# Kernel optimization log

Hardware: AMD Instinct MI355X
Metric: run time of the kernel (lower is better)

The kernel has to match this reference:

```python
import jax, jax.numpy as jnp
import numpy as np

STRIDE = 1
PAD = 1

def setup_inputs() -> dict:
    key = jax.random.key(0)
    k1, k2 = jax.random.split(key)
    x = jax.random.normal(k1, (32, 128, 56, 56), dtype=jnp.float32)
    W = jax.random.normal(k2, (256, 128, 3, 3), dtype=jnp.float32)
    b = jnp.zeros((256,), dtype=jnp.float32)
    return {"x": x, "W": W, "b": b}

def reference(x, W, b):
    # Faithful conv2d: NCHW input, OIHW weight, stride 1, pad 1, plus bias.
    out = jax.lax.conv_general_dilated(
        x, W,
        window_strides=(STRIDE, STRIDE),
        padding=((PAD, PAD), (PAD, PAD)),
        dimension_numbers=("NCHW", "OIHW", "NCHW"),
    )
    return out + b[None, :, None, None]
```

## Files before the change

kernel.cpp:

```cpp
#include <hip/hip_runtime.h>
#include <hip/hip_bf16.h>
#include <cstdint>
#include <cstddef>

#define NB   32
#define CIN  128
#define HWP  3136
#define KOC  256
#define NRS  9
#define PROW 3364
#define WINR 384
#define AEL  12288

typedef __attribute__((ext_vector_type(8))) short  short8;
typedef __attribute__((ext_vector_type(4))) short  short4v;
typedef __attribute__((ext_vector_type(4))) float  float4v;

__device__ __forceinline__ unsigned short f2bf(float f) {
    union { float f; unsigned int u; } v; v.f = f;
    unsigned int u = v.u;
    u = u + 0x7fffu + ((u >> 16) & 1u);
    return (unsigned short)(u >> 16);
}

__global__ __launch_bounds__(256) void prep_kernel(const float* __restrict__ W,
                                                   unsigned short* __restrict__ wt2,
                                                   const float* __restrict__ x,
                                                   unsigned short* __restrict__ xt) {
    __shared__ unsigned short lds[32 * 260];
    int blk = blockIdx.x;
    int t   = threadIdx.x;

    if (blk < 1152) {
        int idx  = blk * 256 + t;
        int e    = idx & 7;
        int lr   = (idx >> 3) & 15;
        int quad = (idx >> 7) & 3;
        int i    = (idx >> 9) & 3;
        int wm   = (idx >> 11) & 1;
        int rem  = idx >> 12;
        int s    = rem % 3;
        int q    = rem / 3;
        int ot   = q & 1;
        int r    = (q >> 1) % 3;
        int ck   = q / 6;
        int rs   = r * 3 + s;
        int oc = ot * 128 + wm * 64 + i * 16 + lr;
        int c  = ck * 32 + quad * 8 + e;
        wt2[idx] = f2bf(W[((size_t)oc * CIN + c) * NRS + rs]);
        return;
    }

    if (blk >= 2816) {
        int g = (blk - 2816) * 256 + t;
        int slab = g / 228;
        int gi   = g - slab * 228;
        int row;
        if (gi < 59)       row = gi;
        else if (gi < 169) { int k = gi - 59;
                             row = 115 + 58 * (k >> 1) + (k & 1); }
        else               row = 3305 + (gi - 169);
        unsigned short* gr = xt + (size_t)slab * (PROW * 32) + (size_t)row * 32;
        short8 z = (short8)0;
        *(short8*)(gr +  0) = z;
        *(short8*)(gr +  8) = z;
        *(short8*)(gr + 16) = z;
        *(short8*)(gr + 24) = z;
        return;
    }

    int b    = blk - 1152;
    int tile = b % 13;
    int ck   = (b / 13) & 3;
    int n    = b / 52;
    int hw0  = tile * 256;
    int wv   = t >> 6;
    int lane = t & 63;

    const float* src = x + ((size_t)(n * CIN + ck * 32)) * HWP;
    #pragma unroll
    for (int pass = 0; pass < 8; ++pass) {
        int c  = pass * 4 + wv;
        int hw = hw0 + lane * 4;
        if (hw < HWP) {
            float4v v = *(const float4v*)(src + (size_t)c * HWP + hw);
            short4v s4;
            #pragma unroll
            for (int k = 0; k < 4; ++k) s4[k] = (short)f2bf(v[k]);
            *(short4v*)(&lds[c * 260 + lane * 4]) = s4;
        }
    }
    __syncthreads();

    int sub = t & 3;
    int hwl = t >> 2;
    unsigned short* dst = xt + ((size_t)(n * 4 + ck)) * PROW * 32;
    #pragma unroll
    for (int pass = 0; pass < 4; ++pass) {
        int hl = pass * 64 + hwl;
        int hw = hw0 + hl;
        if (hw < HWP) {
            short8 v;
            #pragma unroll
            for (int j = 0; j < 8; ++j)
                v[j] = (short)lds[(sub * 8 + j) * 260 + hl];
            int pr = hw + 59 + 2 * (hw / 56);
            *(short8*)(dst + (size_t)pr * 32 + sub * 8) = v;
        }
    }
}

__device__ __forceinline__ void stage_A(const unsigned short* src,
                                        unsigned short* lbase,
                                        int wv, int lane) {
    #pragma unroll
    for (int it = 0; it < 3; ++it) {
        int c0 = it * 512 + wv * 64;
        __builtin_amdgcn_global_load_lds(
            (const __attribute__((address_space(1))) void*)(src + (size_t)(c0 + lane) * 8),
            (__attribute__((address_space(3))) void*)(lbase + (size_t)c0 * 8), 16, 0, 0);
    }
}

__device__ __forceinline__ void stage_B(const unsigned short* gwin,
                                        unsigned short* lbase,
                                        int wv, int lane) {
    #pragma unroll
    for (int it = 0; it < 3; ++it) {
        int blk = it * 8 + wv;
        int s   = blk * 64 + lane;
        int r   = s >> 2;
        int q   = s & 3;
        int qs  = q ^ ((r >> 1) & 3);
        __builtin_amdgcn_global_load_lds(
            (const __attribute__((address_space(1))) void*)(gwin + r * 32 + qs * 8),
            (__attribute__((address_space(3))) void*)(lbase + (size_t)blk * 512), 16, 0, 0);
    }
}

__device__ __forceinline__ short8 ldb(const char* lb, int r, int quad) {
    int q = quad ^ ((r >> 1) & 3);
    return *(const short8*)(lb + r * 64 + q * 16);
}

__global__ __launch_bounds__(512, 2) void gemm_kernel(const unsigned short* __restrict__ xt,
                                                      const unsigned short* __restrict__ wt2,
                                                      const float* __restrict__ bias,
                                                      float* __restrict__ out) {
    __shared__ unsigned short lds[49152];

    int bx = blockIdx.x;
    int ot = bx & 1;
    int n  = (bx >> 1) & 31;
    int pt = bx >> 6;
    int p0 = pt * 256;

    int t    = threadIdx.x;
    int wv   = t >> 6;
    int lane = t & 63;
    int lr   = lane & 15;
    int quad = lane >> 4;
    int wm   = wv >> 2;
    int wn   = wv & 3;

    int prbase = p0 + 2 * (p0 / 56);

    int rb[4];
    #pragma unroll
    for (int j = 0; j < 4; ++j) {
        int hw  = p0 + wn * 64 + j * 16 + lr;
        int hwc = hw < HWP ? hw : (HWP - 1);
        rb[j] = hwc + 59 + 2 * (hwc / 56) - prbase;
    }

    const unsigned short* xb = xt + (size_t)n * 4 * PROW * 32;
    const unsigned short* wb = wt2 + ot * AEL;

    float4v acc[4][4];
    #pragma unroll
    for (int i = 0; i < 4; ++i)
        #pragma unroll
        for (int j = 0; j < 4; ++j)
            acc[i][j] = (float4v){0.f, 0.f, 0.f, 0.f};

    stage_A(wb, lds, wv, lane);
    stage_B(xb + (size_t)prbase * 32, lds + 24576, wv, lane);
    __syncthreads();

    for (int ck = 0; ck < 4; ++ck) {
        for (int r = 0; r < 3; ++r) {
            int g = ck * 3 + r;
            if (g < 11) {
                int r2  = (r == 2) ? 0 : r + 1;
                int ck2 = (r == 2) ? ck + 1 : ck;
                stage_A(wb + (size_t)ck2 * 73728 + (size_t)r2 * 24576,
                        lds + ((g + 1) & 1) * AEL, wv, lane);
            }
            if (r == 2 && ck < 3)
                stage_B(xb + (size_t)(ck + 1) * (PROW * 32) + (size_t)prbase * 32,
                        lds + 24576 + ((ck + 1) & 1) * AEL, wv, lane);

            const unsigned short* A = lds + (g & 1) * AEL + wm * 2048 + lane * 8;
            const char* lbB = (const char*)(lds + 24576 + (ck & 1) * AEL);
            int sh0 = (r - 1) * 58;

            #pragma unroll
            for (int s = 0; s < 3; ++s) {
                int shift = sh0 + s - 1;
                short8 af[4];
                #pragma unroll
                for (int i = 0; i < 4; ++i)
                    af[i] = *(const short8*)(A + s * 4096 + i * 512);
                short8 bcur = ldb(lbB, rb[0] + shift, quad);
                #pragma unroll
                for (int j = 0; j < 4; ++j) {
                    short8 bnext;
                    if (j < 3) bnext = ldb(lbB, rb[j + 1] + shift, quad);
                    #pragma unroll
                    for (int i = 0; i < 4; ++i)
                        acc[i][j] = __builtin_amdgcn_mfma_f32_16x16x32_bf16(
                            af[i], bcur, acc[i][j], 0, 0, 0);
                    if (j < 3) bcur = bnext;
                }
            }
            __syncthreads();
        }
    }

    float* orow = out + (size_t)n * KOC * HWP;
    #pragma unroll
    for (int i = 0; i < 4; ++i) {
        #pragma unroll
        for (int rr = 0; rr < 4; ++rr) {
            int oc = ot * 128 + wm * 64 + i * 16 + quad * 4 + rr;
            float bi = bias[oc];
            #pragma unroll
            for (int j = 0; j < 4; ++j) {
                int hw = p0 + wn * 64 + j * 16 + lr;
                if (hw < HWP)
                    orow[(size_t)oc * HWP + hw] = acc[i][j][rr] + bi;
            }
        }
    }
}

__global__ void naive_kernel(const float* __restrict__ x, const float* __restrict__ W,
                             const float* __restrict__ b, float* __restrict__ out) {
    size_t idx = (size_t)blockIdx.x * 256 + threadIdx.x;
    if (idx >= (size_t)NB * KOC * HWP) return;
    int w0 = (int)(idx % 56);
    int h0 = (int)((idx / 56) % 56);
    int k  = (int)((idx / HWP) % KOC);
    int n  = (int)(idx / ((size_t)HWP * KOC));
    float acc = b[k];
    for (int c = 0; c < CIN; ++c) {
        const float* xr = x + ((size_t)n * CIN + c) * HWP;
        const float* wr = W + ((size_t)k * CIN + c) * NRS;
        for (int r = 0; r < 3; ++r) {
            int h = h0 + r - 1;
            if ((unsigned)h >= 56u) continue;
            for (int s = 0; s < 3; ++s) {
                int w = w0 + s - 1;
                if ((unsigned)w >= 56u) continue;
                acc += xr[h * 56 + w] * wr[r * 3 + s];
            }
        }
    }
    out[idx] = acc;
}

extern "C" void kernel_launch(void* const* d_in, const int* in_sizes, int n_in,
                              void* d_out, int out_size, void* d_ws, size_t ws_size,
                              hipStream_t stream) {
    const float* x  = (const float*)d_in[0];
    const float* W  = (const float*)d_in[1];
    const float* b  = (const float*)d_in[2];
    float* out = (float*)d_out;

    const size_t wt_elems = (size_t)NRS * 4 * 2 * 2 * 4 * 4 * 16 * 8;
    const size_t xt_elems = (size_t)NB * 4 * PROW * 32 + (size_t)WINR * 32;
    const size_t need = (wt_elems + xt_elems) * sizeof(unsigned short);

    if (ws_size < need) {
        size_t total = (size_t)NB * KOC * HWP;
        naive_kernel<<<(unsigned)((total + 255) / 256), 256, 0, stream>>>(x, W, b, out);
        return;
    }

    unsigned short* wt2 = (unsigned short*)d_ws;
    unsigned short* xt  = wt2 + wt_elems;

    prep_kernel<<<1152 + NB * 4 * 13 + 114, 256, 0, stream>>>(W, wt2, x, xt);
    gemm_kernel<<<13 * 32 * 2, 512, 0, stream>>>(xt, wt2, b, out);
}
```

Before: 219.6 us.

## Compute all 256 output channels per block to reuse staged input tiles

Each block now covers all 256 output channels instead of splitting them into two halves across blocks, so every input window is loaded once rather than twice. The weight layout in the prep kernel is reordered to match, the A staging doubles in size, and each wave holds an 8x4 accumulator tile. Raising the wave priority around the MFMA loop is also added. In exchange the grid shrinks to 416 blocks, LDS per block rises to 144 KB and register pressure roughly doubles, which may lower occupancy or cause spills.

```diff
diff --git a/kernel.cpp b/kernel.cpp
--- a/kernel.cpp
+++ b/kernel.cpp
@@ -9,8 +9,9 @@
 #define KOC  256
 #define NRS  9
 #define PROW 3364
-#define WINR 384
-#define AEL  12288
+#define GUARD 256
+#define AEL  24576
+#define BEL  12288
 
 typedef __attribute__((ext_vector_type(8))) short  short8;
 typedef __attribute__((ext_vector_type(4))) short  short4v;
@@ -36,18 +37,15 @@
         int e    = idx & 7;
         int lr   = (idx >> 3) & 15;
         int quad = (idx >> 7) & 3;
-        int i    = (idx >> 9) & 3;
-        int wm   = (idx >> 11) & 1;
-        int rem  = idx >> 12;
-        int s    = rem % 3;
-        int q    = rem / 3;
-        int ot   = q & 1;
-        int r    = (q >> 1) % 3;
-        int ck   = q / 6;
-        int rs   = r * 3 + s;
-        int oc = ot * 128 + wm * 64 + i * 16 + lr;
+        int i4   = (idx >> 9) & 3;
+        int w4   = (idx >> 11) & 3;
+        int q13  = idx >> 13;
+        int s    = q13 % 3;
+        int r    = (q13 / 3) % 3;
+        int ck   = q13 / 9;
+        int oc = w4 * 64 + i4 * 16 + lr;
         int c  = ck * 32 + quad * 8 + e;
-        wt2[idx] = f2bf(W[((size_t)oc * CIN + c) * NRS + rs]);
+        wt2[idx] = f2bf(W[((size_t)oc * CIN + c) * NRS + r * 3 + s]);
         return;
     }
 
@@ -114,7 +112,7 @@
                                         unsigned short* lbase,
                                         int wv, int lane) {
     #pragma unroll
-    for (int it = 0; it < 3; ++it) {
+    for (int it = 0; it < 6; ++it) {
         int c0 = it * 512 + wv * 64;
         __builtin_amdgcn_global_load_lds(
             (const __attribute__((address_space(1))) void*)(src + (size_t)(c0 + lane) * 8),
@@ -147,12 +145,11 @@
                                                       const unsigned short* __restrict__ wt2,
                                                       const float* __restrict__ bias,
                                                       float* __restrict__ out) {
-    __shared__ unsigned short lds[49152];
+    __shared__ unsigned short lds[73728];
 
     int bx = blockIdx.x;
-    int ot = bx & 1;
-    int n  = (bx >> 1) & 31;
-    int pt = bx >> 6;
+    int n  = bx & 31;
+    int pt = bx >> 5;
     int p0 = pt * 256;
 
     int t    = threadIdx.x;
@@ -160,7 +157,7 @@
     int lane = t & 63;
     int lr   = lane & 15;
     int quad = lane >> 4;
-    int wm   = wv >> 2;
+    int ocg  = wv >> 2;
     int wn   = wv & 3;
 
     int prbase = p0 + 2 * (p0 / 56);
@@ -174,17 +171,16 @@
     }
 
     const unsigned short* xb = xt + (size_t)n * 4 * PROW * 32;
-    const unsigned short* wb = wt2 + ot * AEL;
-
-    float4v acc[4][4];
-    #pragma unroll
-    for (int i = 0; i < 4; ++i)
+
+    float4v acc[8][4];
+    #pragma unroll
+    for (int i = 0; i < 8; ++i)
         #pragma unroll
         for (int j = 0; j < 4; ++j)
             acc[i][j] = (float4v){0.f, 0.f, 0.f, 0.f};
 
-    stage_A(wb, lds, wv, lane);
-    stage_B(xb + (size_t)prbase * 32, lds + 24576, wv, lane);
+    stage_A(wt2, lds, wv, lane);
+    stage_B(xb + (size_t)prbase * 32, lds + 49152, wv, lane);
     __syncthreads();
 
     for (int ck = 0; ck < 4; ++ck) {
@@ -193,35 +189,37 @@
             if (g < 11) {
                 int r2  = (r == 2) ? 0 : r + 1;
                 int ck2 = (r == 2) ? ck + 1 : ck;
-                stage_A(wb + (size_t)ck2 * 73728 + (size_t)r2 * 24576,
+                stage_A(wt2 + (size_t)ck2 * 73728 + (size_t)r2 * AEL,
                         lds + ((g + 1) & 1) * AEL, wv, lane);
             }
             if (r == 2 && ck < 3)
                 stage_B(xb + (size_t)(ck + 1) * (PROW * 32) + (size_t)prbase * 32,
-                        lds + 24576 + ((ck + 1) & 1) * AEL, wv, lane);
-
-            const unsigned short* A = lds + (g & 1) * AEL + wm * 2048 + lane * 8;
-            const char* lbB = (const char*)(lds + 24576 + (ck & 1) * AEL);
+                        lds + 49152 + ((ck + 1) & 1) * BEL, wv, lane);
+
+            const unsigned short* A = lds + (g & 1) * AEL + ocg * 4096 + lane * 8;
+            const char* lbB = (const char*)(lds + 49152 + (ck & 1) * BEL);
             int sh0 = (r - 1) * 58;
 
             #pragma unroll
             for (int s = 0; s < 3; ++s) {
                 int shift = sh0 + s - 1;
-                short8 af[4];
+                short8 bcur = ldb(lbB, rb[0] + shift, quad);
+                short8 af[8];
                 #pragma unroll
-                for (int i = 0; i < 4; ++i)
-                    af[i] = *(const short8*)(A + s * 4096 + i * 512);
-                short8 bcur = ldb(lbB, rb[0] + shift, quad);
+                for (int i = 0; i < 8; ++i)
+                    af[i] = *(const short8*)(A + s * 8192 + (i >> 2) * 2048 + (i & 3) * 512);
+                __builtin_amdgcn_s_setprio(1);
                 #pragma unroll
                 for (int j = 0; j < 4; ++j) {
                     short8 bnext;
                     if (j < 3) bnext = ldb(lbB, rb[j + 1] + shift, quad);
                     #pragma unroll
-                    for (int i = 0; i < 4; ++i)
+                    for (int i = 0; i < 8; ++i)
                         acc[i][j] = __builtin_amdgcn_mfma_f32_16x16x32_bf16(
                             af[i], bcur, acc[i][j], 0, 0, 0);
                     if (j < 3) bcur = bnext;
                 }
+                __builtin_amdgcn_s_setprio(0);
             }
             __syncthreads();
         }
@@ -229,10 +227,10 @@
 
     float* orow = out + (size_t)n * KOC * HWP;
     #pragma unroll
-    for (int i = 0; i < 4; ++i) {
+    for (int i = 0; i < 8; ++i) {
         #pragma unroll
         for (int rr = 0; rr < 4; ++rr) {
-            int oc = ot * 128 + wm * 64 + i * 16 + quad * 4 + rr;
+            int oc = ocg * 128 + i * 16 + quad * 4 + rr;
             float bi = bias[oc];
             #pragma unroll
             for (int j = 0; j < 4; ++j) {
@@ -278,7 +276,7 @@
     float* out = (float*)d_out;
 
     const size_t wt_elems = (size_t)NRS * 4 * 2 * 2 * 4 * 4 * 16 * 8;
-    const size_t xt_elems = (size_t)NB * 4 * PROW * 32 + (size_t)WINR * 32;
+    const size_t xt_elems = (size_t)NB * 4 * PROW * 32 + (size_t)GUARD * 32;
     const size_t need = (wt_elems + xt_elems) * sizeof(unsigned short);
 
     if (ws_size < need) {
@@ -291,5 +289,5 @@
     unsigned short* xt  = wt2 + wt_elems;
 
     prep_kernel<<<1152 + NB * 4 * 13 + 114, 256, 0, stream>>>(W, wt2, x, xt);
-    gemm_kernel<<<13 * 32 * 2, 512, 0, stream>>>(xt, wt2, b, out);
-}
+    gemm_kernel<<<13 * 32, 512, 0, stream>>>(xt, wt2, b, out);
+}
```

Result: slower. 246.9 us (+12.4%).
